# Performance work log

Measured on AMD Instinct MI355X. Metric: run time of the kernel, lower is better.

## Reference

```python
import jax, jax.numpy as jnp
import numpy as np

B, S, D = 8, 2048, 256
H, HD = 4, 64  # num_heads, head_size; H*HD == D


def setup_inputs() -> dict:
    key = jax.random.key(0)
    ks = jax.random.split(key, 9)
    scale = 0.02
    return {
        "x": jax.random.normal(ks[0], (B, S, D), dtype=jnp.float32),
        "Wq": jax.random.normal(ks[1], (D, H * HD), dtype=jnp.float32) * scale,
        "bq": jnp.zeros((H * HD,), dtype=jnp.float32),
        "Wk": jax.random.normal(ks[2], (D, H * HD), dtype=jnp.float32) * scale,
        "bk": jnp.zeros((H * HD,), dtype=jnp.float32),
        "Wv": jax.random.normal(ks[3], (D, H * HD), dtype=jnp.float32) * scale,
        "bv": jnp.zeros((H * HD,), dtype=jnp.float32),
        "Wo": jax.random.normal(ks[4], (H * HD, D), dtype=jnp.float32) * scale,
        "bo": jnp.zeros((D,), dtype=jnp.float32),
    }


def _split_heads(t):
    # [B, S, H*HD] -> [B, H, S, HD]
    b, s, _ = t.shape
    return t.reshape(b, s, H, HD).transpose(0, 2, 1, 3)


def reference(x, Wq, bq, Wk, bk, Wv, bv, Wo, bo):
    q = _split_heads(x @ Wq + bq)
    k = _split_heads(x @ Wk + bk)
    v = _split_heads(x @ Wv + bv)
    scores = jnp.einsum("bhqd,bhkd->bhqk", q, k) / jnp.sqrt(jnp.float32(HD))
    weights = jax.nn.softmax(scores, axis=-1)
    attn = jnp.einsum("bhqk,bhkd->bhqd", weights, v)  # [B, H, S, HD]
    concat = attn.transpose(0, 2, 1, 3).reshape(x.shape[0], -1, H * HD)
    return concat @ Wo + bo
```

## Files before the change

### kernel.cpp

```cpp
#include <hip/hip_runtime.h>
#include <hip/hip_bf16.h>

namespace {

constexpr int B_ = 8, S = 2048, D = 256, H = 4, HD = 64;
constexpr int M = B_ * S;

typedef __attribute__((ext_vector_type(8))) short bf16x8;
typedef __attribute__((ext_vector_type(4))) short bf16x4;
typedef __attribute__((ext_vector_type(4))) float f32x4;
typedef __attribute__((ext_vector_type(16))) float f32x16;
typedef __attribute__((ext_vector_type(4))) unsigned uint4v;

__device__ inline short f2bf(float x) {
  __hip_bfloat16 h = __float2bfloat16(x);
  short s;
  __builtin_memcpy(&s, &h, 2);
  return s;
}

__device__ inline f32x4 mfma16(bf16x8 a, bf16x8 b, f32x4 c) {
  return __builtin_amdgcn_mfma_f32_16x16x32_bf16(a, b, c, 0, 0, 0);
}
__device__ inline f32x16 mfma32(bf16x8 a, bf16x8 b, f32x16 c) {
  return __builtin_amdgcn_mfma_f32_32x32x16_bf16(a, b, c, 0, 0, 0);
}

__device__ inline float exp2a(float x) {
  float r;
  asm("v_exp_f32 %0, %1" : "=v"(r) : "v"(x));
  return r;
}

__device__ inline unsigned cvtpk(float lo, float hi) {
  unsigned r;
  asm("v_cvt_pk_bf16_f32 %0, %1, %2" : "=v"(r) : "v"(lo), "v"(hi));
  return r;
}

__device__ inline bf16x4 pk4(float a, float b, float c, float d) {
  unsigned lo = cvtpk(a, b), hi = cvtpk(c, d);
  uint2 u{lo, hi};
  bf16x4 r;
  __builtin_memcpy(&r, &u, 8);
  return r;
}

__device__ inline bf16x8 ld_cvt8(const float* p) {
  float4 a = *(const float4*)p;
  float4 b = *(const float4*)(p + 4);
  uint4v u = {cvtpk(a.x, a.y), cvtpk(a.z, a.w), cvtpk(b.x, b.y), cvtpk(b.z, b.w)};
  bf16x8 r;
  __builtin_memcpy(&r, &u, 16);
  return r;
}

__global__ __launch_bounds__(256) void prep_w_kernel(
    const float* __restrict__ Wq, const float* __restrict__ Wk,
    const float* __restrict__ Wv, const float* __restrict__ Wo,
    short* __restrict__ WqT, short* __restrict__ WkT,
    short* __restrict__ WvT, short* __restrict__ WoT) {
  const int blk = blockIdx.x, t = threadIdx.x;
  const int wq = blk >> 4, n0 = (blk & 15) * 16;
  const float* W = wq == 0 ? Wq : wq == 1 ? Wk : wq == 2 ? Wv : Wo;
  short* Wt = wq == 0 ? WqT : wq == 1 ? WkT : wq == 2 ? WvT : WoT;
#pragma unroll
  for (int j4 = 0; j4 < 4; ++j4) {
    float4 v = *(const float4*)(W + (size_t)t * 256 + n0 + j4 * 4);
    Wt[(n0 + j4 * 4 + 0) * 256 + t] = f2bf(v.x);
    Wt[(n0 + j4 * 4 + 1) * 256 + t] = f2bf(v.y);
    Wt[(n0 + j4 * 4 + 2) * 256 + t] = f2bf(v.z);
    Wt[(n0 + j4 * 4 + 3) * 256 + t] = f2bf(v.w);
  }
}

__global__ __launch_bounds__(256) void gemm_qkv_kernel(
    const float* __restrict__ x,
    const short* __restrict__ WqT, const short* __restrict__ WkT,
    const short* __restrict__ WvT,
    const float* __restrict__ bq, const float* __restrict__ bk,
    const float* __restrict__ bv,
    short* __restrict__ Qo, short* __restrict__ Ko, short* __restrict__ Vt) {
  const int bx = blockIdx.x;
  const int which = blockIdx.y;
  const short* Wt = which == 0 ? WqT : which == 1 ? WkT : WvT;
  const float* bias = which == 0 ? bq : which == 1 ? bk : bv;

  __shared__ short Xs[2][64 * 32];
  __shared__ short Ws[2][256 * 32];

  const int tid = threadIdx.x;
  const int wid = tid >> 6, lane = tid & 63;
  const int l15 = lane & 15, l4 = lane >> 4;
  const int nt0 = wid * 4;

  const float* xsrc = x + ((size_t)(bx * 64 + (tid >> 2))) * 256 + (tid & 3) * 8;
  const short* wsrc = Wt + ((size_t)(tid >> 2)) * 256 + (tid & 3) * 8;
  short* xdst0 = &Xs[0][tid * 8];
  short* xdst1 = &Xs[1][tid * 8];
  short* wdst0 = &Ws[0][tid * 8];
  short* wdst1 = &Ws[1][tid * 8];

  bf16x8 xr, wr[4];
  xr = ld_cvt8(xsrc);
#pragma unroll
  for (int p = 0; p < 4; ++p) wr[p] = *(const bf16x8*)(wsrc + (size_t)p * 64 * 256);
  *(bf16x8*)xdst0 = xr;
#pragma unroll
  for (int p = 0; p < 4; ++p) *(bf16x8*)(wdst0 + p * 2048) = wr[p];
  __syncthreads();

  f32x4 acc[4][4];
#pragma unroll
  for (int i = 0; i < 4; ++i)
#pragma unroll
    for (int mh = 0; mh < 4; ++mh) acc[i][mh] = f32x4{0.f, 0.f, 0.f, 0.f};

  for (int ks = 0; ks < 8; ++ks) {
    const int cur = ks & 1;
    if (ks < 7) {
      xr = ld_cvt8(xsrc + (ks + 1) * 32);
#pragma unroll
      for (int p = 0; p < 4; ++p)
        wr[p] = *(const bf16x8*)(wsrc + (size_t)p * 64 * 256 + (ks + 1) * 32);
    }
    bf16x8 wf[4], xf[4];
#pragma unroll
    for (int i = 0; i < 4; ++i)
      wf[i] = *(const bf16x8*)&Ws[cur][((nt0 + i) * 16 + l15) * 32 + l4 * 8];
#pragma unroll
    for (int mh = 0; mh < 4; ++mh)
      xf[mh] = *(const bf16x8*)&Xs[cur][(mh * 16 + l15) * 32 + l4 * 8];
    if (which == 2) {
#pragma unroll
      for (int i = 0; i < 4; ++i)
#pragma unroll
        for (int mh = 0; mh < 4; ++mh)
          acc[i][mh] = mfma16(xf[mh], wf[i], acc[i][mh]);
    } else {
#pragma unroll
      for (int i = 0; i < 4; ++i)
#pragma unroll
        for (int mh = 0; mh < 4; ++mh)
          acc[i][mh] = mfma16(wf[i], xf[mh], acc[i][mh]);
    }
    if (ks < 7) {
      short* xd = (cur ? xdst0 : xdst1);
      short* wd = (cur ? wdst0 : wdst1);
      *(bf16x8*)xd = xr;
#pragma unroll
      for (int p = 0; p < 4; ++p) *(bf16x8*)(wd + p * 2048) = wr[p];
    }
    __syncthreads();
  }

  if (which == 2) {
    const int m0 = bx * 64 + l4 * 4;
#pragma unroll
    for (int i = 0; i < 4; ++i) {
      const int n = (nt0 + i) * 16 + l15;
      const float bi = bias[n];
      const int h = n >> 6, d = n & 63;
#pragma unroll
      for (int mh = 0; mh < 4; ++mh) {
        const int m = m0 + mh * 16;
        const int bb = m >> 11, s0 = m & 2047;
        bf16x4 r = pk4(acc[i][mh][0] + bi, acc[i][mh][1] + bi,
                       acc[i][mh][2] + bi, acc[i][mh][3] + bi);
        *(bf16x4*)(Vt + (((size_t)bb * H + h) * HD + d) * S + s0) = r;
      }
    }
  } else {
    const float scale = which == 0 ? 0.18033688011112042f : 1.0f;
    short* outp = which == 0 ? Qo : Ko;
#pragma unroll
    for (int i = 0; i < 4; ++i) {
      const int n0 = (nt0 + i) * 16 + l4 * 4;
      float4 bi = *(const float4*)(bias + n0);
      const int h = n0 >> 6, d0 = n0 & 63;
#pragma unroll
      for (int mh = 0; mh < 4; ++mh) {
        const int m = bx * 64 + mh * 16 + l15;
        const int bb = m >> 11, s = m & 2047;
        bf16x4 r = pk4((acc[i][mh][0] + bi.x) * scale, (acc[i][mh][1] + bi.y) * scale,
                       (acc[i][mh][2] + bi.z) * scale, (acc[i][mh][3] + bi.w) * scale);
        *(bf16x4*)(outp + (((size_t)bb * H + h) * S + s) * HD + d0) = r;
      }
    }
  }
}

__global__ __launch_bounds__(256) void gemm_out_kernel(
    const short* __restrict__ Abf, const short* __restrict__ WoT,
    const float* __restrict__ bo, float* __restrict__ out) {
  const int bx = blockIdx.x;
  __shared__ short Xs[2][64 * 32];
  __shared__ short Ws[2][256 * 32];

  const int tid = threadIdx.x;
  const int wid = tid >> 6, lane = tid & 63;
  const int l15 = lane & 15, l4 = lane >> 4;
  const int nt0 = wid * 4;

  const short* xsrc = Abf + ((size_t)(bx * 64 + (tid >> 2))) * 256 + (tid & 3) * 8;
  const short* wsrc = WoT + ((size_t)(tid >> 2)) * 256 + (tid & 3) * 8;
  short* xdst0 = &Xs[0][tid * 8];
  short* xdst1 = &Xs[1][tid * 8];
  short* wdst0 = &Ws[0][tid * 8];
  short* wdst1 = &Ws[1][tid * 8];

  bf16x8 xr, wr[4];
  xr = *(const bf16x8*)xsrc;
#pragma unroll
  for (int p = 0; p < 4; ++p) wr[p] = *(const bf16x8*)(wsrc + (size_t)p * 64 * 256);
  *(bf16x8*)xdst0 = xr;
#pragma unroll
  for (int p = 0; p < 4; ++p) *(bf16x8*)(wdst0 + p * 2048) = wr[p];
  __syncthreads();

  f32x4 acc[4][4];
#pragma unroll
  for (int i = 0; i < 4; ++i)
#pragma unroll
    for (int mh = 0; mh < 4; ++mh) acc[i][mh] = f32x4{0.f, 0.f, 0.f, 0.f};

  for (int ks = 0; ks < 8; ++ks) {
    const int cur = ks & 1;
    if (ks < 7) {
      xr = *(const bf16x8*)(xsrc + (ks + 1) * 32);
#pragma unroll
      for (int p = 0; p < 4; ++p)
        wr[p] = *(const bf16x8*)(wsrc + (size_t)p * 64 * 256 + (ks + 1) * 32);
    }
    bf16x8 wf[4], xf[4];
#pragma unroll
    for (int i = 0; i < 4; ++i)
      wf[i] = *(const bf16x8*)&Ws[cur][((nt0 + i) * 16 + l15) * 32 + l4 * 8];
#pragma unroll
    for (int mh = 0; mh < 4; ++mh)
      xf[mh] = *(const bf16x8*)&Xs[cur][(mh * 16 + l15) * 32 + l4 * 8];
#pragma unroll
    for (int i = 0; i < 4; ++i)
#pragma unroll
      for (int mh = 0; mh < 4; ++mh)
        acc[i][mh] = mfma16(wf[i], xf[mh], acc[i][mh]);
    if (ks < 7) {
      short* xd = (cur ? xdst0 : xdst1);
      short* wd = (cur ? wdst0 : wdst1);
      *(bf16x8*)xd = xr;
#pragma unroll
      for (int p = 0; p < 4; ++p) *(bf16x8*)(wd + p * 2048) = wr[p];
    }
    __syncthreads();
  }

#pragma unroll
  for (int i = 0; i < 4; ++i) {
    const int n0 = (nt0 + i) * 16 + l4 * 4;
    float4 bi = *(const float4*)(bo + n0);
#pragma unroll
    for (int mh = 0; mh < 4; ++mh) {
      const int m = bx * 64 + mh * 16 + l15;
      float4 r;
      r.x = acc[i][mh][0] + bi.x;
      r.y = acc[i][mh][1] + bi.y;
      r.z = acc[i][mh][2] + bi.z;
      r.w = acc[i][mh][3] + bi.w;
      *(float4*)(out + (size_t)m * 256 + n0) = r;
    }
  }
}

__global__ __launch_bounds__(256) void attn_kernel6(
    const short* __restrict__ Q, const short* __restrict__ K,
    const short* __restrict__ VT, short* __restrict__ Abf) {
  const int lin = blockIdx.x;
  const int bh = lin & 31;
  const int qt = lin >> 5;
  const int tid = threadIdx.x, wid = tid >> 6, lane = tid & 63;
  const int q31 = lane & 31, h = lane >> 5;

  __shared__ short Ks[2][64 * 128];
  __shared__ short Vs[2][64 * 128];

  const short* Kg = K + (size_t)bh * S * HD;
  const short* Vg = VT + (size_t)bh * HD * S;
  const int qrow = qt * 128 + wid * 32;

  const short* Qg = Q + ((size_t)bh * S + qrow + q31) * HD + h * 8;
  bf16x8 qf[4];
#pragma unroll
  for (int ds = 0; ds < 4; ++ds) qf[ds] = *(const bf16x8*)(Qg + ds * 16);

  const int srow = tid >> 2;
  const int scol = (tid & 3) * 16;
  const int swz = (srow & 15) * 8;
  const int c0 = scol ^ swz;
  const int c1 = (scol + 8) ^ swz;

  const int fs = (lane & 15) * 8;
  int kcol[4];
#pragma unroll
  for (int ds = 0; ds < 4; ++ds) kcol[ds] = (ds * 16 + h * 8) ^ fs;

  bf16x8 kr0, kr1, vr0, vr1;
  kr0 = *(const bf16x8*)(Kg + (size_t)srow * HD + scol);
  kr1 = *(const bf16x8*)(Kg + (size_t)srow * HD + scol + 8);
  vr0 = *(const bf16x8*)(Vg + (size_t)srow * S + scol);
  vr1 = *(const bf16x8*)(Vg + (size_t)srow * S + scol + 8);
  *(bf16x8*)&Ks[0][srow * 128 + c0] = kr0;
  *(bf16x8*)&Ks[0][srow * 128 + c1] = kr1;
  *(bf16x8*)&Vs[0][srow * 128 + c0] = vr0;
  *(bf16x8*)&Vs[0][srow * 128 + c1] = vr1;
  __syncthreads();

  f32x16 o0, o1;
#pragma unroll
  for (int i = 0; i < 16; ++i) { o0[i] = 0.f; o1[i] = 0.f; }
  float lacc = 0.f;

  for (int kt = 0; kt < S / 64; ++kt) {
    const int cur = kt & 1;
    if (kt + 1 < S / 64) {
      const short* Kn = Kg + (size_t)(kt + 1) * 64 * HD;
      const short* Vn = Vg + (size_t)(kt + 1) * 64;
      kr0 = *(const bf16x8*)(Kn + (size_t)srow * HD + scol);
      kr1 = *(const bf16x8*)(Kn + (size_t)srow * HD + scol + 8);
      vr0 = *(const bf16x8*)(Vn + (size_t)srow * S + scol);
      vr1 = *(const bf16x8*)(Vn + (size_t)srow * S + scol + 8);
    }

    f32x16 sc0, sc1;
#pragma unroll
    for (int i = 0; i < 16; ++i) { sc0[i] = 0.f; sc1[i] = 0.f; }
    __builtin_amdgcn_s_setprio(1);
#pragma unroll
    for (int ds = 0; ds < 4; ++ds) {
      bf16x8 k0 = *(const bf16x8*)&Ks[cur][(q31)*128 + kcol[ds]];
      bf16x8 k1 = *(const bf16x8*)&Ks[cur][(32 + q31) * 128 + kcol[ds]];
      sc0 = mfma32(k0, qf[ds], sc0);
      sc1 = mfma32(k1, qf[ds], sc1);
    }
    __builtin_amdgcn_s_setprio(0);

    bf16x8 pB[4];
#pragma unroll
    for (int win = 0; win < 2; ++win) {
      const f32x16& sc = win ? sc1 : sc0;
      float p[16];
      float a0 = 0.f, a1 = 0.f, a2 = 0.f, a3 = 0.f;
#pragma unroll
      for (int r = 0; r < 16; r += 4) {
        p[r + 0] = exp2a(sc[r + 0]);
        p[r + 1] = exp2a(sc[r + 1]);
        p[r + 2] = exp2a(sc[r + 2]);
        p[r + 3] = exp2a(sc[r + 3]);
        a0 += p[r + 0]; a1 += p[r + 1]; a2 += p[r + 2]; a3 += p[r + 3];
      }
      lacc += (a0 + a1) + (a2 + a3);
      unsigned w[8];
#pragma unroll
      for (int i = 0; i < 8; ++i) w[i] = cvtpk(p[2 * i], p[2 * i + 1]);
      unsigned x0 = w[0], y0 = w[2];
      unsigned x1 = w[1], y1 = w[3];
      unsigned x2 = w[4], y2 = w[6];
      unsigned x3 = w[5], y3 = w[7];
      asm("v_permlane32_swap_b32 %0, %1" : "+v"(x0), "+v"(y0));
      asm("v_permlane32_swap_b32 %0, %1" : "+v"(x1), "+v"(y1));
      asm("v_permlane32_swap_b32 %0, %1" : "+v"(x2), "+v"(y2));
      asm("v_permlane32_swap_b32 %0, %1" : "+v"(x3), "+v"(y3));
      uint4v u0 = {x0, x1, y0, y1};
      uint4v u1 = {x2, x3, y2, y3};
      __builtin_memcpy(&pB[win * 2 + 0], &u0, 16);
      __builtin_memcpy(&pB[win * 2 + 1], &u1, 16);
    }

    __builtin_amdgcn_s_setprio(1);
#pragma unroll
    for (int kq = 0; kq < 4; ++kq) {
      bf16x8 v0 = *(const bf16x8*)&Vs[cur][(q31)*128 + kcol[kq]];
      bf16x8 v1 = *(const bf16x8*)&Vs[cur][(32 + q31) * 128 + kcol[kq]];
      o0 = mfma32(v0, pB[kq], o0);
      o1 = mfma32(v1, pB[kq], o1);
    }
    __builtin_amdgcn_s_setprio(0);

    if (kt + 1 < S / 64) {
      const int nxt = cur ^ 1;
      *(bf16x8*)&Ks[nxt][srow * 128 + c0] = kr0;
      *(bf16x8*)&Ks[nxt][srow * 128 + c1] = kr1;
      *(bf16x8*)&Vs[nxt][srow * 128 + c0] = vr0;
      *(bf16x8*)&Vs[nxt][srow * 128 + c1] = vr1;
    }
    __syncthreads();
  }

  const float lall = lacc + __shfl_xor(lacc, 32);
  const float inv = 1.0f / lall;
  const int b = bh >> 2, hh = bh & 3;
  short* ap = Abf + ((size_t)b * S + qrow + q31) * 256 + hh * 64;
#pragma unroll
  for (int dt = 0; dt < 2; ++dt) {
    const f32x16& o = dt ? o1 : o0;
#pragma unroll
    for (int g = 0; g < 4; ++g) {
      const int d0 = dt * 32 + 8 * g + 4 * h;
      bf16x4 r = pk4(o[4 * g + 0] * inv, o[4 * g + 1] * inv,
                     o[4 * g + 2] * inv, o[4 * g + 3] * inv);
      *(bf16x4*)(ap + d0) = r;
    }
  }
}

}

extern "C" void kernel_launch(void* const* d_in, const int* in_sizes, int n_in,
                              void* d_out, int out_size, void* d_ws, size_t ws_size,
                              hipStream_t stream) {
  const float* x  = (const float*)d_in[0];
  const float* Wq = (const float*)d_in[1];
  const float* bq = (const float*)d_in[2];
  const float* Wk = (const float*)d_in[3];
  const float* bk = (const float*)d_in[4];
  const float* Wv = (const float*)d_in[5];
  const float* bv = (const float*)d_in[6];
  const float* Wo = (const float*)d_in[7];
  const float* bo = (const float*)d_in[8];
  float* out = (float*)d_out;

  const size_t per = (size_t)M * D;
  short* WqT = (short*)d_ws;
  short* WkT = WqT + 256 * 256;
  short* WvT = WkT + 256 * 256;
  short* WoT = WvT + 256 * 256;
  short* Qbf = WoT + 256 * 256;
  short* Kbf = Qbf + per;
  short* Vt  = Kbf + per;
  short* Abf = Vt + per;

  prep_w_kernel<<<64, 256, 0, stream>>>(Wq, Wk, Wv, Wo, WqT, WkT, WvT, WoT);
  gemm_qkv_kernel<<<dim3(256, 3), 256, 0, stream>>>(x, WqT, WkT, WvT, bq, bk, bv,
                                                    Qbf, Kbf, Vt);
  attn_kernel6<<<512, 256, 0, stream>>>(Qbf, Kbf, Vt, Abf);
  gemm_out_kernel<<<256, 256, 0, stream>>>(Abf, WoT, bo, out);
}
```

Before: 89.24 us.

## Software-pipeline attention: overlap QK^T of next tile with PV of previous

Restructures the attention loop so that in each iteration the QK^T MFMAs for tile kt are interleaved with the PV MFMAs for tile kt-1, with prologue and epilogue handling the first and last tiles. The softmax denominator is now computed on the matrix unit with an extra MFMA against a ones vector instead of scalar adds and a cross-lane shuffle. The aim is to hide exp and pack latency behind matrix work and cut VALU work. In exchange it adds one MFMA per step, an extra barrier per iteration, and more register pressure from keeping pB live across iterations.

```diff
diff --git a/kernel.cpp b/kernel.cpp
--- a/kernel.cpp
+++ b/kernel.cpp
@@ -271,7 +271,7 @@
   }
 }
 
-__global__ __launch_bounds__(256) void attn_kernel6(
+__global__ __launch_bounds__(256) void attn_kernel7(
     const short* __restrict__ Q, const short* __restrict__ K,
     const short* __restrict__ VT, short* __restrict__ Abf) {
   const int lin = blockIdx.x;
@@ -279,6 +279,7 @@
   const int qt = lin >> 5;
   const int tid = threadIdx.x, wid = tid >> 6, lane = tid & 63;
   const int q31 = lane & 31, h = lane >> 5;
+  constexpr int NT = S / 64;
 
   __shared__ short Ks[2][64 * 128];
   __shared__ short Vs[2][64 * 128];
@@ -291,6 +292,10 @@
   bf16x8 qf[4];
 #pragma unroll
   for (int ds = 0; ds < 4; ++ds) qf[ds] = *(const bf16x8*)(Qg + ds * 16);
+
+  bf16x8 ones;
+#pragma unroll
+  for (int i = 0; i < 8; ++i) ones[i] = (short)0x3F80;
 
   const int srow = tid >> 2;
   const int scol = (tid & 3) * 16;
@@ -312,16 +317,69 @@
   *(bf16x8*)&Ks[0][srow * 128 + c1] = kr1;
   *(bf16x8*)&Vs[0][srow * 128 + c0] = vr0;
   *(bf16x8*)&Vs[0][srow * 128 + c1] = vr1;
+  {
+    const short* Kn = Kg + (size_t)64 * HD;
+    const short* Vn = Vg + 64;
+    kr0 = *(const bf16x8*)(Kn + (size_t)srow * HD + scol);
+    kr1 = *(const bf16x8*)(Kn + (size_t)srow * HD + scol + 8);
+    vr0 = *(const bf16x8*)(Vn + (size_t)srow * S + scol);
+    vr1 = *(const bf16x8*)(Vn + (size_t)srow * S + scol + 8);
+  }
   __syncthreads();
 
-  f32x16 o0, o1;
-#pragma unroll
-  for (int i = 0; i < 16; ++i) { o0[i] = 0.f; o1[i] = 0.f; }
-  float lacc = 0.f;
-
-  for (int kt = 0; kt < S / 64; ++kt) {
-    const int cur = kt & 1;
-    if (kt + 1 < S / 64) {
+  f32x16 o0, o1, lsum;
+#pragma unroll
+  for (int i = 0; i < 16; ++i) { o0[i] = 0.f; o1[i] = 0.f; lsum[i] = 0.f; }
+  bf16x8 pB[4];
+
+#define EXPPACK(S0, S1)                                               \
+  {                                                                   \
+    _Pragma("unroll") for (int win = 0; win < 2; ++win) {             \
+      const f32x16& sc = win ? (S1) : (S0);                           \
+      float p[16];                                                    \
+      _Pragma("unroll") for (int r = 0; r < 16; ++r)                  \
+          p[r] = exp2a(sc[r]);                                        \
+      unsigned w[8];                                                  \
+      _Pragma("unroll") for (int i = 0; i < 8; ++i)                   \
+          w[i] = cvtpk(p[2 * i], p[2 * i + 1]);                       \
+      unsigned x0 = w[0], y0 = w[2], x1 = w[1], y1 = w[3];            \
+      unsigned x2 = w[4], y2 = w[6], x3 = w[5], y3 = w[7];            \
+      asm("v_permlane32_swap_b32 %0, %1" : "+v"(x0), "+v"(y0));       \
+      asm("v_permlane32_swap_b32 %0, %1" : "+v"(x1), "+v"(y1));       \
+      asm("v_permlane32_swap_b32 %0, %1" : "+v"(x2), "+v"(y2));       \
+      asm("v_permlane32_swap_b32 %0, %1" : "+v"(x3), "+v"(y3));       \
+      uint4v u0 = {x0, x1, y0, y1};                                   \
+      uint4v u1 = {x2, x3, y2, y3};                                   \
+      __builtin_memcpy(&pB[win * 2 + 0], &u0, 16);                    \
+      __builtin_memcpy(&pB[win * 2 + 1], &u1, 16);                    \
+    }                                                                 \
+  }
+
+  {
+    f32x16 sc0, sc1;
+#pragma unroll
+    for (int i = 0; i < 16; ++i) { sc0[i] = 0.f; sc1[i] = 0.f; }
+    __builtin_amdgcn_s_setprio(1);
+#pragma unroll
+    for (int ds = 0; ds < 4; ++ds) {
+      bf16x8 k0 = *(const bf16x8*)&Ks[0][(q31)*128 + kcol[ds]];
+      bf16x8 k1 = *(const bf16x8*)&Ks[0][(32 + q31) * 128 + kcol[ds]];
+      sc0 = mfma32(k0, qf[ds], sc0);
+      sc1 = mfma32(k1, qf[ds], sc1);
+    }
+    __builtin_amdgcn_s_setprio(0);
+    EXPPACK(sc0, sc1);
+    __syncthreads();
+    *(bf16x8*)&Ks[1][srow * 128 + c0] = kr0;
+    *(bf16x8*)&Ks[1][srow * 128 + c1] = kr1;
+    *(bf16x8*)&Vs[1][srow * 128 + c0] = vr0;
+    *(bf16x8*)&Vs[1][srow * 128 + c1] = vr1;
+    __syncthreads();
+  }
+
+  for (int kt = 1; kt < NT; ++kt) {
+    const int cur = kt & 1, prv = cur ^ 1;
+    if (kt + 1 < NT) {
       const short* Kn = Kg + (size_t)(kt + 1) * 64 * HD;
       const short* Vn = Vg + (size_t)(kt + 1) * 64;
       kr0 = *(const bf16x8*)(Kn + (size_t)srow * HD + scol);
@@ -333,6 +391,7 @@
     f32x16 sc0, sc1;
 #pragma unroll
     for (int i = 0; i < 16; ++i) { sc0[i] = 0.f; sc1[i] = 0.f; }
+
     __builtin_amdgcn_s_setprio(1);
 #pragma unroll
     for (int ds = 0; ds < 4; ++ds) {
@@ -340,63 +399,41 @@
       bf16x8 k1 = *(const bf16x8*)&Ks[cur][(32 + q31) * 128 + kcol[ds]];
       sc0 = mfma32(k0, qf[ds], sc0);
       sc1 = mfma32(k1, qf[ds], sc1);
+      bf16x8 v0 = *(const bf16x8*)&Vs[prv][(q31)*128 + kcol[ds]];
+      bf16x8 v1 = *(const bf16x8*)&Vs[prv][(32 + q31) * 128 + kcol[ds]];
+      o0 = mfma32(v0, pB[ds], o0);
+      o1 = mfma32(v1, pB[ds], o1);
+      lsum = mfma32(ones, pB[ds], lsum);
     }
     __builtin_amdgcn_s_setprio(0);
 
-    bf16x8 pB[4];
-#pragma unroll
-    for (int win = 0; win < 2; ++win) {
-      const f32x16& sc = win ? sc1 : sc0;
-      float p[16];
-      float a0 = 0.f, a1 = 0.f, a2 = 0.f, a3 = 0.f;
-#pragma unroll
-      for (int r = 0; r < 16; r += 4) {
-        p[r + 0] = exp2a(sc[r + 0]);
-        p[r + 1] = exp2a(sc[r + 1]);
-        p[r + 2] = exp2a(sc[r + 2]);
-        p[r + 3] = exp2a(sc[r + 3]);
-        a0 += p[r + 0]; a1 += p[r + 1]; a2 += p[r + 2]; a3 += p[r + 3];
-      }
-      lacc += (a0 + a1) + (a2 + a3);
-      unsigned w[8];
-#pragma unroll
-      for (int i = 0; i < 8; ++i) w[i] = cvtpk(p[2 * i], p[2 * i + 1]);
-      unsigned x0 = w[0], y0 = w[2];
-      unsigned x1 = w[1], y1 = w[3];
-      unsigned x2 = w[4], y2 = w[6];
-      unsigned x3 = w[5], y3 = w[7];
-      asm("v_permlane32_swap_b32 %0, %1" : "+v"(x0), "+v"(y0));
-      asm("v_permlane32_swap_b32 %0, %1" : "+v"(x1), "+v"(y1));
-      asm("v_permlane32_swap_b32 %0, %1" : "+v"(x2), "+v"(y2));
-      asm("v_permlane32_swap_b32 %0, %1" : "+v"(x3), "+v"(y3));
-      uint4v u0 = {x0, x1, y0, y1};
-      uint4v u1 = {x2, x3, y2, y3};
-      __builtin_memcpy(&pB[win * 2 + 0], &u0, 16);
-      __builtin_memcpy(&pB[win * 2 + 1], &u1, 16);
-    }
-
+    EXPPACK(sc0, sc1);
+    __syncthreads();
+    if (kt + 1 < NT) {
+      *(bf16x8*)&Ks[prv][srow * 128 + c0] = kr0;
+      *(bf16x8*)&Ks[prv][srow * 128 + c1] = kr1;
+      *(bf16x8*)&Vs[prv][srow * 128 + c0] = vr0;
+      *(bf16x8*)&Vs[prv][srow * 128 + c1] = vr1;
+    }
+    __syncthreads();
+  }
+
+  {
+    const int cur = (NT - 1) & 1;
     __builtin_amdgcn_s_setprio(1);
 #pragma unroll
-    for (int kq = 0; kq < 4; ++kq) {
-      bf16x8 v0 = *(const bf16x8*)&Vs[cur][(q31)*128 + kcol[kq]];
-      bf16x8 v1 = *(const bf16x8*)&Vs[cur][(32 + q31) * 128 + kcol[kq]];
-      o0 = mfma32(v0, pB[kq], o0);
-      o1 = mfma32(v1, pB[kq], o1);
+    for (int ds = 0; ds < 4; ++ds) {
+      bf16x8 v0 = *(const bf16x8*)&Vs[cur][(q31)*128 + kcol[ds]];
+      bf16x8 v1 = *(const bf16x8*)&Vs[cur][(32 + q31) * 128 + kcol[ds]];
+      o0 = mfma32(v0, pB[ds], o0);
+      o1 = mfma32(v1, pB[ds], o1);
+      lsum = mfma32(ones, pB[ds], lsum);
     }
     __builtin_amdgcn_s_setprio(0);
-
-    if (kt + 1 < S / 64) {
-      const int nxt = cur ^ 1;
-      *(bf16x8*)&Ks[nxt][srow * 128 + c0] = kr0;
-      *(bf16x8*)&Ks[nxt][srow * 128 + c1] = kr1;
-      *(bf16x8*)&Vs[nxt][srow * 128 + c0] = vr0;
-      *(bf16x8*)&Vs[nxt][srow * 128 + c1] = vr1;
-    }
-    __syncthreads();
-  }
-
-  const float lall = lacc + __shfl_xor(lacc, 32);
-  const float inv = 1.0f / lall;
+  }
+#undef EXPPACK
+
+  const float inv = 1.0f / lsum[0];
   const int b = bh >> 2, hh = bh & 3;
   short* ap = Abf + ((size_t)b * S + qrow + q31) * 256 + hh * 64;
 #pragma unroll
@@ -441,6 +478,6 @@
   prep_w_kernel<<<64, 256, 0, stream>>>(Wq, Wk, Wv, Wo, WqT, WkT, WvT, WoT);
   gemm_qkv_kernel<<<dim3(256, 3), 256, 0, stream>>>(x, WqT, WkT, WvT, bq, bk, bv,
                                                     Qbf, Kbf, Vt);
-  attn_kernel6<<<512, 256, 0, stream>>>(Qbf, Kbf, Vt, Abf);
+  attn_kernel7<<<512, 256, 0, stream>>>(Qbf, Kbf, Vt, Abf);
   gemm_out_kernel<<<256, 256, 0, stream>>>(Abf, WoT, bo, out);
 }
```

After: 88.30 us. Within noise of the previous version (-1.1%).
